# Kernel optimization log

Hardware: AMD Instinct MI355X
Metric: run time of the kernel (lower is better)

Reference implementation:

```python
import jax, jax.numpy as jnp
import numpy as np

N, C = 2, 256
GH0, GW0 = 40, 40
GH1, GW1 = 40, 40
STRIDE, TOPK = 2, 8
TEMP, THRESH, BORDER = 0.1, 0.2, 2
H0, W0 = GH0 * STRIDE, GW0 * STRIDE
H1, W1 = GH1 * STRIDE, GW1 * STRIDE
K4 = TOPK * STRIDE * STRIDE
# create_meshgrid(2,2) flattened: entries (x, y) in row-major (y outer) order
GRID = jnp.array([[0, 0], [1, 0], [0, 1], [1, 1]], dtype=jnp.int32)


def map_indices(idx, size0, size1):
    # idx: (n, G0, topk) coarse indices into image1 coarse grid
    row = idx[..., None] // size1[1] * STRIDE + GRID[:, 1]
    col = idx[..., None] % size1[1] * STRIDE + GRID[:, 0]
    fine = row * (size1[1] * STRIDE) + col  # (n, G0, topk, 4)
    n = idx.shape[0]
    fine = fine.reshape(n, size0[0], 1, size0[1], 1, -1)
    fine = jnp.broadcast_to(fine, (n, size0[0], STRIDE, size0[1], STRIDE, fine.shape[-1]))
    return fine.reshape(n, size0[0] * size0[1] * STRIDE * STRIDE, -1)


def remove_border_one_side(idx, br, size):
    h, w = size
    pos = jnp.arange(h * w)
    r, c = pos // w, pos % w
    border = (r < br) | (r >= h - br) | (c < br) | (c >= w - br)
    return jnp.where(border[None, :], 0, idx)


def unpatchify(x, grid, stride):
    n, g, s2, c = x.shape
    gh, gw = grid
    x = x.reshape(n, gh, gw, stride, stride, c)
    x = jnp.transpose(x, (0, 5, 1, 3, 2, 4))
    return x.reshape(n, c, gh * stride, gw * stride)


def fused_heatmaps(x0, x1, a01, a10, ind0_f, ind1_f):
    s01 = jnp.einsum('ngqc,ngkc->ngqk', x0, a01) / C  # (n, G0, 4, K4)
    s10 = jnp.einsum('ngqc,ngkc->ngqk', x1, a10) / C
    h01 = jax.nn.softmax(s01 / TEMP, axis=-1)
    h10 = jax.nn.softmax(s10 / TEMP, axis=-1)
    h01 = h01.reshape(N, GH0, GW0, STRIDE, STRIDE, K4)
    h01 = jnp.transpose(h01, (0, 1, 3, 2, 4, 5)).reshape(N, H0 * W0, K4)
    h10 = h10.reshape(N, GH1, GW1, STRIDE, STRIDE, K4)
    h10 = jnp.transpose(h10, (0, 5, 1, 3, 2, 4)).reshape(N, K4, H1 * W1)
    # dense scatter + gather mutual fusion (as in the torch code)
    b = jnp.arange(N)[:, None, None]
    l1 = jnp.arange(H1 * W1)[None, None, :]
    Z0 = jnp.zeros((N, H0 * W0, H1 * W1), h10.dtype).at[b, ind1_f, l1].set(h10)
    new_h01 = h01 * jnp.take_along_axis(Z0, ind0_f, axis=-1)
    l0 = jnp.arange(H0 * W0)[None, :, None]
    Z1 = jnp.zeros((N, H0 * W0, H1 * W1), h01.dtype).at[b, l0, ind0_f].set(h01)
    new_h10 = h10 * jnp.take_along_axis(Z1, ind1_f, axis=-2)
    return new_h01, new_h10


def coarse_matching(h01, h10, ind0_f, ind1_f):
    score = jnp.max(h01, axis=-1)                 # (n, L0)
    sub0 = jnp.argmax(h01, axis=-1)               # (n, L0)
    j_best = jnp.take_along_axis(ind0_f, sub0[..., None], axis=-1)[..., 0]
    sub1 = jnp.argmax(h10, axis=-2)               # (n, L1)
    i_best = jnp.take_along_axis(ind1_f, sub1[:, None, :], axis=-2)[:, 0, :]
    j_best = remove_border_one_side(j_best, BORDER, (H1, W1))
    i_best = remove_border_one_side(i_best, BORDER, (H0, W0))
    biproj = jnp.take_along_axis(i_best, j_best, axis=-1)
    mask = biproj == jnp.arange(H0 * W0)[None, :]
    mask = mask.at[:, 0].set(False)
    mask = mask & (score > THRESH)
    scores = jnp.where(mask, score, 0.0)
    return mask, j_best, scores


def setup_inputs() -> dict:
    key = jax.random.key(0)
    ks = jax.random.split(key, 6)
    return {
        'x0': jax.random.normal(ks[0], (N, GH0 * GW0, 4, C), jnp.float32),
        'x1': jax.random.normal(ks[1], (N, GH1 * GW1, 4, C), jnp.float32),
        'attended0_to_1': jax.random.normal(ks[2], (N, GH0 * GW0, K4, C), jnp.float32),
        'attended1_to_0': jax.random.normal(ks[3], (N, GH1 * GW1, K4, C), jnp.float32),
        'x0_prior': jax.random.normal(ks[4], (N, C, GH0, GW0), jnp.float32),
        'x1_prior': jax.random.normal(ks[5], (N, C, GH1, GW1), jnp.float32),
    }


def reference(x0, x1, attended0_to_1, attended1_to_0, x0_prior, x1_prior):
    p0 = x0_prior.reshape(N, C, GH0 * GW0)
    p1 = x1_prior.reshape(N, C, GH1 * GW1)
    sim = jnp.einsum('nci,ncj->nij', p0, p1) / C  # (n, G0, G1)
    _, i01 = jax.lax.top_k(sim, TOPK)                              # (n, G0, topk)
    _, i10 = jax.lax.top_k(jnp.swapaxes(sim, -2, -1), TOPK)        # (n, G1, topk)
    ind0_f = map_indices(i01, (GH0, GW0), (GH1, GW1))              # (n, L0, K4)
    ind1_f = jnp.swapaxes(map_indices(i10, (GH1, GW1), (GH0, GW0)), -2, -1)  # (n, K4, L1)
    h01, h10 = fused_heatmaps(x0, x1, attended0_to_1, attended1_to_0, ind0_f, ind1_f)
    mask, j_best, scores = coarse_matching(jax.lax.stop_gradient(h01), jax.lax.stop_gradient(h10), ind0_f, ind1_f)
    x0_8x = unpatchify(x0, (GH0, GW0), STRIDE)
    x1_8x = unpatchify(x1, (GH1, GW1), STRIDE)
    return h01, h10, scores, j_best, mask, x0_8x, x1_8x
```

## Files before the change

kernel.cpp:

```cpp
#include <hip/hip_runtime.h>


#define N_B   2
#define C_DIM 256
#define G0N   1600
#define GW    40
#define L0N   6400
#define W_F   80
#define TK    8

__global__ __launch_bounds__(256) void k_sim(const float* __restrict__ p0,
                                             const float* __restrict__ p1,
                                             float* __restrict__ sim,
                                             float* __restrict__ simT) {
  const int n  = blockIdx.z;
  const int i0 = blockIdx.y * 128;
  const int j0 = blockIdx.x * 128;
  const float* A = p0 + (size_t)n * C_DIM * G0N;
  const float* B = p1 + (size_t)n * C_DIM * G0N;
  __shared__ float As[16][128];
  __shared__ float Bs[16][128];
  const int t  = threadIdx.x;
  const int tx = t & 15, ty = t >> 4;
  const int lf = t & 31;
  const int lr = t >> 5;

  float acc[8][8];
#pragma unroll
  for (int a = 0; a < 8; ++a)
#pragma unroll
    for (int b = 0; b < 8; ++b) acc[a][b] = 0.f;

  int ia = i0 + lf * 4; if (ia > G0N - 4) ia = G0N - 4;
  int ja = j0 + lf * 4; if (ja > G0N - 4) ja = G0N - 4;

  for (int kc = 0; kc < C_DIM; kc += 16) {
#pragma unroll
    for (int p = 0; p < 2; ++p) {
      int row = lr + p * 8;
      int c = kc + row;
      float4 av = *(const float4*)(A + (size_t)c * G0N + ia);
      float4 bv = *(const float4*)(B + (size_t)c * G0N + ja);
      *(float4*)&As[row][lf * 4] = av;
      *(float4*)&Bs[row][lf * 4] = bv;
    }
    __syncthreads();
#pragma unroll
    for (int k = 0; k < 16; ++k) {
      float a[8], b[8];
      *(float4*)&a[0] = *(const float4*)&As[k][ty * 8];
      *(float4*)&a[4] = *(const float4*)&As[k][ty * 8 + 4];
      *(float4*)&b[0] = *(const float4*)&Bs[k][tx * 8];
      *(float4*)&b[4] = *(const float4*)&Bs[k][tx * 8 + 4];
#pragma unroll
      for (int ii = 0; ii < 8; ++ii)
#pragma unroll
        for (int jj = 0; jj < 8; ++jj) acc[ii][jj] += a[ii] * b[jj];
    }
    __syncthreads();
  }

  float* simn  = sim  + (size_t)n * G0N * G0N;
  float* simTn = simT + (size_t)n * G0N * G0N;
#pragma unroll
  for (int ii = 0; ii < 8; ++ii) {
    int i = i0 + ty * 8 + ii;
    if (i < G0N) {
#pragma unroll
      for (int j4 = 0; j4 < 2; ++j4) {
        int j = j0 + tx * 8 + j4 * 4;
        if (j < G0N) {
          float4 v = make_float4(acc[ii][j4*4], acc[ii][j4*4+1], acc[ii][j4*4+2], acc[ii][j4*4+3]);
          *(float4*)(simn + (size_t)i * G0N + j) = v;
        }
      }
    }
  }
#pragma unroll
  for (int jj = 0; jj < 8; ++jj) {
    int j = j0 + tx * 8 + jj;
    if (j < G0N) {
#pragma unroll
      for (int i4 = 0; i4 < 2; ++i4) {
        int i = i0 + ty * 8 + i4 * 4;
        if (i < G0N) {
          float4 v = make_float4(acc[i4*4][jj], acc[i4*4+1][jj], acc[i4*4+2][jj], acc[i4*4+3][jj]);
          *(float4*)(simTn + (size_t)j * G0N + i) = v;
        }
      }
    }
  }
}

__global__ __launch_bounds__(256) void k_topk(const float* __restrict__ sim,
                                              const float* __restrict__ simT,
                                              int* __restrict__ i01,
                                              int* __restrict__ i10) {
  int wid  = (blockIdx.x * 256 + threadIdx.x) >> 6;
  int lane = threadIdx.x & 63;
  int dir  = wid / (N_B * G0N);
  int r    = wid - dir * (N_B * G0N);
  const float* row = (dir ? simT : sim) + (size_t)r * G0N;
  int* out = (dir ? i10 : i01) + r * TK;

  float v[25];
#pragma unroll
  for (int tt = 0; tt < 25; ++tt) v[tt] = row[lane + 64 * tt];

#pragma unroll 1
  for (int k = 0; k < TK; ++k) {
    float best = -3.4e38f; int bidx = 0x7fffffff;
#pragma unroll
    for (int tt = 0; tt < 25; ++tt) {
      if (v[tt] > best) { best = v[tt]; bidx = lane + 64 * tt; }
    }
#pragma unroll
    for (int off = 1; off < 64; off <<= 1) {
      float ov = __shfl_xor(best, off);
      int   oi = __shfl_xor(bidx, off);
      if (ov > best || (ov == best && oi < bidx)) { best = ov; bidx = oi; }
    }
    if (lane == 0) out[k] = bidx;
#pragma unroll
    for (int tt = 0; tt < 25; ++tt)
      if (lane + 64 * tt == bidx) v[tt] = -3.4e38f;
  }
}

__global__ __launch_bounds__(128) void k_heat(const float* __restrict__ x,
                                              const float* __restrict__ att,
                                              float* __restrict__ hpre) {
  const int ng = blockIdx.x;
  const float* xp = x   + (size_t)ng * 4  * C_DIM;
  const float* ap = att + (size_t)ng * 32 * C_DIM;
  __shared__ float xs[4 * C_DIM];
  __shared__ float as[32][260];
  const int t = threadIdx.x;
#pragma unroll
  for (int j = 0; j < 16; ++j) {
    int f = t + j * 128;
    float4 v = *(const float4*)(ap + (size_t)f * 4);
    *(float4*)&as[f >> 6][(f & 63) * 4] = v;
  }
#pragma unroll
  for (int j = 0; j < 2; ++j) {
    int f = t + j * 128;
    *(float4*)&xs[f * 4] = *(const float4*)(xp + (size_t)f * 4);
  }
  __syncthreads();
  const int k4 = t & 31, q = t >> 5;
  float acc = 0.f;
#pragma unroll
  for (int c4 = 0; c4 < 64; ++c4) {
    float4 a  = *(const float4*)&as[k4][c4 * 4];
    float4 xv = *(const float4*)&xs[q * C_DIM + c4 * 4];
    acc += a.x * xv.x + a.y * xv.y + a.z * xv.z + a.w * xv.w;
  }
  float l = (acc * (1.0f / 256.0f)) / 0.1f;
  float m = l;
#pragma unroll
  for (int off = 1; off < 32; off <<= 1) m = fmaxf(m, __shfl_xor(m, off));
  float e = expf(l - m);
  float s = e;
#pragma unroll
  for (int off = 1; off < 32; off <<= 1) s += __shfl_xor(s, off);
  hpre[(size_t)ng * 128 + q * 32 + k4] = e / s;
}

__global__ __launch_bounds__(256) void k_fuse01(const float* __restrict__ h01p,
                                                const float* __restrict__ h10p,
                                                const int* __restrict__ i01,
                                                const int* __restrict__ i10,
                                                float* __restrict__ h01_out,
                                                float* __restrict__ score_ws,
                                                int* __restrict__ jbest_ws,
                                                float* __restrict__ jbest_out) {
  int idx = blockIdx.x * 8 + (threadIdx.x >> 5);
  int k4  = threadIdx.x & 31;
  int n = idx / L0N, l0 = idx - n * L0N;
  int r0 = l0 / W_F, c0 = l0 - r0 * W_F;
  int g0 = (r0 >> 1) * GW + (c0 >> 1);
  int q0 = ((r0 & 1) << 1) | (c0 & 1);
  int k = k4 >> 2, g = k4 & 3;
  int jc = i01[(n * G0N + g0) * TK + k];
  const int* row10 = i10 + (n * G0N + jc) * TK;
  int kf = -1;
#pragma unroll
  for (int kp = 0; kp < 8; ++kp) if (row10[kp] == g0) kf = kp;
  float m = 0.f;
  if (kf >= 0) m = h10p[((n * G0N + jc) * 4 + g) * 32 + kf * 4 + q0];
  float h = h01p[((n * G0N + g0) * 4 + q0) * 32 + k4];
  float val = h * m;
  h01_out[(size_t)idx * 32 + k4] = val;

  float best = val; int bi = k4;
#pragma unroll
  for (int off = 1; off < 32; off <<= 1) {
    float ov = __shfl_xor(best, off);
    int   oi = __shfl_xor(bi, off);
    if (ov > best || (ov == best && oi < bi)) { best = ov; bi = oi; }
  }
  if (k4 == 0) {
    score_ws[idx] = best;
    int kB = bi >> 2, gB = bi & 3;
    int jcB = i01[(n * G0N + g0) * TK + kB];
    int jrow = jcB / GW;
    int jb = ((jrow * 2 + (gB >> 1)) * W_F) + (jcB - jrow * GW) * 2 + (gB & 1);
    if (r0 < 2 || r0 >= W_F - 2 || c0 < 2 || c0 >= W_F - 2) jb = 0;
    jbest_ws[idx]  = jb;
    jbest_out[idx] = (float)jb;
  }
}

__global__ __launch_bounds__(256) void k_fuse10(const float* __restrict__ h01p,
                                                const float* __restrict__ h10p,
                                                const int* __restrict__ i01,
                                                const int* __restrict__ i10,
                                                float* __restrict__ h10_out,
                                                int* __restrict__ ibest_ws) {
  int idx = blockIdx.x * 8 + (threadIdx.x >> 5);
  int k4  = threadIdx.x & 31;
  int n = idx / L0N, l1 = idx - n * L0N;
  int r1 = l1 / W_F, c1 = l1 - r1 * W_F;
  int g1 = (r1 >> 1) * GW + (c1 >> 1);
  int q1 = ((r1 & 1) << 1) | (c1 & 1);
  int k = k4 >> 2, g = k4 & 3;
  int ic = i10[(n * G0N + g1) * TK + k];
  const int* row01 = i01 + (n * G0N + ic) * TK;
  int kf = -1;
#pragma unroll
  for (int kp = 0; kp < 8; ++kp) if (row01[kp] == g1) kf = kp;
  float m = 0.f;
  if (kf >= 0) m = h01p[((n * G0N + ic) * 4 + g) * 32 + kf * 4 + q1];
  float h = h10p[((n * G0N + g1) * 4 + q1) * 32 + k4];
  float val = h * m;
  h10_out[((size_t)n * 32 + k4) * L0N + l1] = val;

  float best = val; int bi = k4;
#pragma unroll
  for (int off = 1; off < 32; off <<= 1) {
    float ov = __shfl_xor(best, off);
    int   oi = __shfl_xor(bi, off);
    if (ov > best || (ov == best && oi < bi)) { best = ov; bi = oi; }
  }
  if (k4 == 0) {
    int kB = bi >> 2, gB = bi & 3;
    int icB = i10[(n * G0N + g1) * TK + kB];
    int irow = icB / GW;
    int ib = ((irow * 2 + (gB >> 1)) * W_F) + (icB - irow * GW) * 2 + (gB & 1);
    if (r1 < 2 || r1 >= W_F - 2 || c1 < 2 || c1 >= W_F - 2) ib = 0;
    ibest_ws[idx] = ib;
  }
}

__global__ __launch_bounds__(256) void k_final(const float* __restrict__ score_ws,
                                               const int* __restrict__ jbest_ws,
                                               const int* __restrict__ ibest_ws,
                                               float* __restrict__ scores_out,
                                               float* __restrict__ mask_out) {
  int idx = blockIdx.x * 256 + threadIdx.x;
  if (idx >= N_B * L0N) return;
  int n = idx / L0N, l0 = idx - n * L0N;
  int jb = jbest_ws[idx];
  float sc = score_ws[idx];
  int biproj = ibest_ws[n * L0N + jb];
  bool mk = (biproj == l0) && (l0 != 0) && (sc > 0.2f);
  scores_out[idx] = mk ? sc : 0.f;
  mask_out[idx]   = mk ? 1.f : 0.f;
}

__global__ __launch_bounds__(256) void k_unpatch(const float* __restrict__ x,
                                                 float* __restrict__ out) {
  __shared__ float tile[32][33];
  int cc0 = blockIdx.x * 32;
  int r   = blockIdx.y;
  int n   = blockIdx.z >> 3;
  int c0  = (blockIdx.z & 7) * 32;
  int t = threadIdx.x;
  int sr = r & 1, ghr = r >> 1;
  int pos = t >> 5, cl = t & 31;
#pragma unroll
  for (int it = 0; it < 4; ++it) {
    int p = pos + it * 8;
    int cc = cc0 + p;
    if (cc < W_F) {
      int gg = ghr * GW + (cc >> 1);
      int qq = (sr << 1) | (cc & 1);
      tile[p][cl] = x[(((size_t)n * G0N + gg) * 4 + qq) * C_DIM + c0 + cl];
    }
  }
  __syncthreads();
  int co = t >> 5, p2 = t & 31;
#pragma unroll
  for (int it = 0; it < 4; ++it) {
    int c = c0 + co + it * 8;
    int cc = cc0 + p2;
    if (cc < W_F)
      out[(((size_t)n * C_DIM + c) * W_F + r) * W_F + cc] = tile[p2][co + it * 8];
  }
}

extern "C" void kernel_launch(void* const* d_in, const int* in_sizes, int n_in,
                              void* d_out, int out_size, void* d_ws, size_t ws_size,
                              hipStream_t stream) {
  const float* x0  = (const float*)d_in[0];
  const float* x1  = (const float*)d_in[1];
  const float* a01 = (const float*)d_in[2];
  const float* a10 = (const float*)d_in[3];
  const float* p0  = (const float*)d_in[4];
  const float* p1  = (const float*)d_in[5];
  float* out = (float*)d_out;

  float* ws       = (float*)d_ws;
  float* sim      = ws;
  float* simT     = ws + 5120000;
  int*   i01      = (int*)(ws + 10240000);
  int*   i10      = (int*)(ws + 10265600);
  float* h01p     = ws + 10291200;
  float* h10p     = ws + 10700800;
  float* score_ws = ws + 11110400;
  int*   jbest_ws = (int*)(ws + 11123200);
  int*   ibest_ws = (int*)(ws + 11136000);

  float* o_h01   = out;
  float* o_h10   = out + 409600;
  float* o_score = out + 819200;
  float* o_jbest = out + 832000;
  float* o_mask  = out + 844800;
  float* o_x08   = out + 857600;
  float* o_x18   = out + 4134400;

  k_sim<<<dim3(13, 13, 2), 256, 0, stream>>>(p0, p1, sim, simT);
  k_topk<<<1600, 256, 0, stream>>>(sim, simT, i01, i10);
  k_heat<<<3200, 128, 0, stream>>>(x0, a01, h01p);
  k_heat<<<3200, 128, 0, stream>>>(x1, a10, h10p);
  k_fuse01<<<1600, 256, 0, stream>>>(h01p, h10p, i01, i10, o_h01, score_ws, jbest_ws, o_jbest);
  k_fuse10<<<1600, 256, 0, stream>>>(h01p, h10p, i01, i10, o_h10, ibest_ws);
  k_final<<<50, 256, 0, stream>>>(score_ws, jbest_ws, ibest_ws, o_score, o_mask);
  k_unpatch<<<dim3(3, 80, 16), 256, 0, stream>>>(x0, o_x08);
  k_unpatch<<<dim3(3, 80, 16), 256, 0, stream>>>(x1, o_x18);
}
```

Baseline: 364.2 us.

## Retile similarity GEMM to 64x64 and merge paired heat/unpatch launches

The similarity GEMM moves from 128x128 tiles with 8x8 per-thread outputs on 338 blocks to 64x64 tiles with 8x4 outputs on 1250 blocks, with a K chunk of 32. Since 1600 divides evenly by 64, the edge clamps and bounds checks are dropped. This gives more blocks and lower register pressure, so the GPU's compute units are better filled. The two k_heat launches and the two k_unpatch launches are each merged into one launch that picks its inputs by block index, removing launch gaps at the cost of less register reuse per thread in the GEMM.

After: 344.4 us. 1.06x faster.

```diff
diff --git a/kernel.cpp b/kernel.cpp
--- a/kernel.cpp
+++ b/kernel.cpp
@@ -9,86 +9,67 @@
 #define W_F   80
 #define TK    8
 
-__global__ __launch_bounds__(256) void k_sim(const float* __restrict__ p0,
+#define KC 32
+__global__ __launch_bounds__(128) void k_sim(const float* __restrict__ p0,
                                              const float* __restrict__ p1,
                                              float* __restrict__ sim,
                                              float* __restrict__ simT) {
   const int n  = blockIdx.z;
-  const int i0 = blockIdx.y * 128;
-  const int j0 = blockIdx.x * 128;
+  const int i0 = blockIdx.y * 64;
+  const int j0 = blockIdx.x * 64;
   const float* A = p0 + (size_t)n * C_DIM * G0N;
   const float* B = p1 + (size_t)n * C_DIM * G0N;
-  __shared__ float As[16][128];
-  __shared__ float Bs[16][128];
+  __shared__ float As[KC][64];
+  __shared__ float Bs[KC][64];
   const int t  = threadIdx.x;
-  const int tx = t & 15, ty = t >> 4;
-  const int lf = t & 31;
-  const int lr = t >> 5;
-
-  float acc[8][8];
-#pragma unroll
-  for (int a = 0; a < 8; ++a)
-#pragma unroll
-    for (int b = 0; b < 8; ++b) acc[a][b] = 0.f;
-
-  int ia = i0 + lf * 4; if (ia > G0N - 4) ia = G0N - 4;
-  int ja = j0 + lf * 4; if (ja > G0N - 4) ja = G0N - 4;
-
-  for (int kc = 0; kc < C_DIM; kc += 16) {
-#pragma unroll
-    for (int p = 0; p < 2; ++p) {
-      int row = lr + p * 8;
-      int c = kc + row;
-      float4 av = *(const float4*)(A + (size_t)c * G0N + ia);
-      float4 bv = *(const float4*)(B + (size_t)c * G0N + ja);
-      *(float4*)&As[row][lf * 4] = av;
-      *(float4*)&Bs[row][lf * 4] = bv;
+  const int tx = t & 15;
+  const int ty = t >> 4;
+
+  float4 acc[8];
+#pragma unroll
+  for (int ii = 0; ii < 8; ++ii) acc[ii] = make_float4(0.f, 0.f, 0.f, 0.f);
+
+  for (int kc = 0; kc < C_DIM; kc += KC) {
+#pragma unroll
+    for (int u = 0; u < 4; ++u) {
+      int f   = t + u * 128;
+      int row = f >> 4;
+      int c4  = (f & 15) * 4;
+      *(float4*)&As[row][c4] = *(const float4*)(A + (size_t)(kc + row) * G0N + i0 + c4);
+      *(float4*)&Bs[row][c4] = *(const float4*)(B + (size_t)(kc + row) * G0N + j0 + c4);
     }
     __syncthreads();
 #pragma unroll
-    for (int k = 0; k < 16; ++k) {
-      float a[8], b[8];
+    for (int k = 0; k < KC; ++k) {
+      __attribute__((aligned(16))) float a[8];
       *(float4*)&a[0] = *(const float4*)&As[k][ty * 8];
       *(float4*)&a[4] = *(const float4*)&As[k][ty * 8 + 4];
-      *(float4*)&b[0] = *(const float4*)&Bs[k][tx * 8];
-      *(float4*)&b[4] = *(const float4*)&Bs[k][tx * 8 + 4];
-#pragma unroll
-      for (int ii = 0; ii < 8; ++ii)
-#pragma unroll
-        for (int jj = 0; jj < 8; ++jj) acc[ii][jj] += a[ii] * b[jj];
+      float4 bv = *(const float4*)&Bs[k][tx * 4];
+#pragma unroll
+      for (int ii = 0; ii < 8; ++ii) {
+        acc[ii].x += a[ii] * bv.x;
+        acc[ii].y += a[ii] * bv.y;
+        acc[ii].z += a[ii] * bv.z;
+        acc[ii].w += a[ii] * bv.w;
+      }
     }
     __syncthreads();
   }
 
   float* simn  = sim  + (size_t)n * G0N * G0N;
   float* simTn = simT + (size_t)n * G0N * G0N;
-#pragma unroll
-  for (int ii = 0; ii < 8; ++ii) {
-    int i = i0 + ty * 8 + ii;
-    if (i < G0N) {
-#pragma unroll
-      for (int j4 = 0; j4 < 2; ++j4) {
-        int j = j0 + tx * 8 + j4 * 4;
-        if (j < G0N) {
-          float4 v = make_float4(acc[ii][j4*4], acc[ii][j4*4+1], acc[ii][j4*4+2], acc[ii][j4*4+3]);
-          *(float4*)(simn + (size_t)i * G0N + j) = v;
-        }
-      }
-    }
-  }
-#pragma unroll
-  for (int jj = 0; jj < 8; ++jj) {
-    int j = j0 + tx * 8 + jj;
-    if (j < G0N) {
-#pragma unroll
-      for (int i4 = 0; i4 < 2; ++i4) {
-        int i = i0 + ty * 8 + i4 * 4;
-        if (i < G0N) {
-          float4 v = make_float4(acc[i4*4][jj], acc[i4*4+1][jj], acc[i4*4+2][jj], acc[i4*4+3][jj]);
-          *(float4*)(simTn + (size_t)j * G0N + i) = v;
-        }
-      }
-    }
+  const int ib = i0 + ty * 8;
+  const int jb = j0 + tx * 4;
+  const float* accf = (const float*)acc;
+#pragma unroll
+  for (int ii = 0; ii < 8; ++ii)
+    *(float4*)(simn + (size_t)(ib + ii) * G0N + jb) = acc[ii];
+#pragma unroll
+  for (int jj = 0; jj < 4; ++jj) {
+    float4 lo = make_float4(accf[0 * 4 + jj], accf[1 * 4 + jj], accf[2 * 4 + jj], accf[3 * 4 + jj]);
+    float4 hi = make_float4(accf[4 * 4 + jj], accf[5 * 4 + jj], accf[6 * 4 + jj], accf[7 * 4 + jj]);
+    *(float4*)(simTn + (size_t)(jb + jj) * G0N + ib)     = lo;
+    *(float4*)(simTn + (size_t)(jb + jj) * G0N + ib + 4) = hi;
   }
 }
 
@@ -127,10 +108,18 @@
   }
 }
 
-__global__ __launch_bounds__(128) void k_heat(const float* __restrict__ x,
-                                              const float* __restrict__ att,
-                                              float* __restrict__ hpre) {
-  const int ng = blockIdx.x;
+__global__ __launch_bounds__(128) void k_heat(const float* __restrict__ x0,
+                                              const float* __restrict__ a01,
+                                              float* __restrict__ h01p,
+                                              const float* __restrict__ x1,
+                                              const float* __restrict__ a10,
+                                              float* __restrict__ h10p) {
+  int bid = blockIdx.x;
+  const float* x   = x0;
+  const float* att = a01;
+  float*       hpre = h01p;
+  int ng = bid;
+  if (bid >= N_B * G0N) { x = x1; att = a10; hpre = h10p; ng = bid - N_B * G0N; }
   const float* xp = x   + (size_t)ng * 4  * C_DIM;
   const float* ap = att + (size_t)ng * 32 * C_DIM;
   __shared__ float xs[4 * C_DIM];
@@ -269,13 +258,19 @@
   mask_out[idx]   = mk ? 1.f : 0.f;
 }
 
-__global__ __launch_bounds__(256) void k_unpatch(const float* __restrict__ x,
-                                                 float* __restrict__ out) {
+__global__ __launch_bounds__(256) void k_unpatch(const float* __restrict__ x0,
+                                                 float* __restrict__ out0,
+                                                 const float* __restrict__ x1,
+                                                 float* __restrict__ out1) {
   __shared__ float tile[32][33];
+  int z = blockIdx.z;
+  const float* x = (z < 16) ? x0 : x1;
+  float* out     = (z < 16) ? out0 : out1;
+  int zz  = z & 15;
   int cc0 = blockIdx.x * 32;
   int r   = blockIdx.y;
-  int n   = blockIdx.z >> 3;
-  int c0  = (blockIdx.z & 7) * 32;
+  int n   = zz >> 3;
+  int c0  = (zz & 7) * 32;
   int t = threadIdx.x;
   int sr = r & 1, ghr = r >> 1;
   int pos = t >> 5, cl = t & 31;
@@ -330,13 +325,11 @@
   float* o_x08   = out + 857600;
   float* o_x18   = out + 4134400;
 
-  k_sim<<<dim3(13, 13, 2), 256, 0, stream>>>(p0, p1, sim, simT);
+  k_sim<<<dim3(25, 25, 2), 128, 0, stream>>>(p0, p1, sim, simT);
   k_topk<<<1600, 256, 0, stream>>>(sim, simT, i01, i10);
-  k_heat<<<3200, 128, 0, stream>>>(x0, a01, h01p);
-  k_heat<<<3200, 128, 0, stream>>>(x1, a10, h10p);
+  k_heat<<<6400, 128, 0, stream>>>(x0, a01, h01p, x1, a10, h10p);
   k_fuse01<<<1600, 256, 0, stream>>>(h01p, h10p, i01, i10, o_h01, score_ws, jbest_ws, o_jbest);
   k_fuse10<<<1600, 256, 0, stream>>>(h01p, h10p, i01, i10, o_h10, ibest_ws);
   k_final<<<50, 256, 0, stream>>>(score_ws, jbest_ws, ibest_ws, o_score, o_mask);
-  k_unpatch<<<dim3(3, 80, 16), 256, 0, stream>>>(x0, o_x08);
-  k_unpatch<<<dim3(3, 80, 16), 256, 0, stream>>>(x1, o_x18);
-}
+  k_unpatch<<<dim3(3, 80, 32), 256, 0, stream>>>(x0, o_x08, x1, o_x18);
+}
```
